# Performance work log

Hardware: AMD Instinct MI355X
Metric: run time of the kernel (lower is better)

Reference implementation:

```python
import jax, jax.numpy as jnp
import numpy as np

N = 192            # image grid size (NxN)
N_SHOTS = 192
N_SAMPLES = 192
TWO_PI = 2.0 * np.pi
PIPE_ITERS = 3     # gpunufft default is ~10; 3 suffices for a CPU-runnable reference


def initialize_2D_radial(n_shots, n_samples):
    """Radial trajectory, k in [-0.5, 0.5), shape (n_shots*n_samples, 2)."""
    angles = np.pi * np.arange(n_shots) / n_shots
    radii = np.linspace(-0.5, 0.5, n_samples, endpoint=False)
    kx = radii[None, :] * np.cos(angles[:, None])
    ky = radii[None, :] * np.sin(angles[:, None])
    return np.stack([kx, ky], axis=-1).reshape(-1, 2).astype(np.float32)


def setup_inputs() -> dict:
    key = jax.random.key(0)
    x = jax.random.normal(key, (2, N, N), dtype=jnp.float32)  # real/imag image
    trajectory = jnp.asarray(initialize_2D_radial(N_SHOTS, N_SAMPLES))  # (M,2)
    return {"x": x, "trajectory": trajectory}


def _mats(traj):
    # Separable NDFT factors: exp(-2pi i k_x * px), exp(-2pi i k_y * py).
    # A: (M, N), B: (M, N); M*N complex64 ~= 57 MB each.
    p = jnp.arange(N, dtype=jnp.float32) - N / 2.0  # centered pixel coords
    A = jnp.exp(-1j * TWO_PI * traj[:, 0:1] * p[None, :])
    B = jnp.exp(-1j * TWO_PI * traj[:, 1:2] * p[None, :])
    return A.astype(jnp.complex64), B.astype(jnp.complex64)


def _op(img, A, B):
    # type-2 NUFFT (exact NDFT): image (N,N) -> kspace (M,)
    t = jnp.einsum('my,xy->mx', B, img)      # contract y first
    return jnp.einsum('mx,mx->m', A, t)


def _adj(d, A, B):
    # type-1 NUFFT adjoint: samples (M,) -> image (N,N)
    return jnp.einsum('mx,my->xy', jnp.conj(A) * d[:, None], jnp.conj(B))


def _pipe_density(A, B):
    # Pipe & Menon iterative density compensation: w <- w / |F F^H w|
    w = jnp.ones(A.shape[0], dtype=jnp.complex64)
    def body(i, w):
        q = _op(_adj(w, A, B), A, B)
        return w / jnp.maximum(jnp.abs(q), 1e-20)
    w = jax.lax.fori_loop(0, PIPE_ITERS, body, w)
    return jnp.abs(w)  # real positive weights


def reference(x, trajectory):
    img = (x[0] + 1j * x[1]).astype(jnp.complex64)  # (N,N) complex image
    A, B = _mats(trajectory)
    # density weights computed from detached trajectory (gpunufft init-time)
    traj_sg = jax.lax.stop_gradient(trajectory)
    Asg, Bsg = _mats(traj_sg)
    w = jax.lax.stop_gradient(_pipe_density(Asg, Bsg))
    kspace = _op(img, A, B)                       # forward NUFFT
    adjoint = _adj(w * kspace, A, B)              # density-compensated adjoint
    return jnp.stack([adjoint.real, adjoint.imag])  # (2,N,N) float32
```

## Files before the change

kernel.cpp:

```cpp
#include <hip/hip_runtime.h>
#include <math.h>


#define MTOT 36864
#define NPIX 192
#define SPLITS 128
#define GRP 64
#define NCH 36
#define PG 64

typedef __attribute__((ext_vector_type(8))) short s16x8;
typedef __attribute__((ext_vector_type(4))) float f32x4;
typedef __attribute__((ext_vector_type(4))) unsigned u32x4;

__device__ __forceinline__ f32x4 mfma_bf16(u32x4 a, u32x4 b, f32x4 c) {
    return __builtin_amdgcn_mfma_f32_16x16x32_bf16(
        __builtin_bit_cast(s16x8, a), __builtin_bit_cast(s16x8, b), c, 0, 0, 0);
}

__device__ __forceinline__ void g2l16(const void* g, void* l) {
    __builtin_amdgcn_global_load_lds(
        (const __attribute__((address_space(1))) void*)g,
        (__attribute__((address_space(3))) void*)l, 16, 0, 0);
}

__device__ __forceinline__ void split_pk(float a, float b, unsigned &hi, unsigned &lo) {
    const unsigned ua = __float_as_uint(a), ub = __float_as_uint(b);
    const unsigned ha = (ua + 0x8000u) & 0xffff0000u;
    const unsigned hb = (ub + 0x8000u) & 0xffff0000u;
    hi = (ha >> 16) | hb;
    const float la = a - __uint_as_float(ha);
    const float lb = b - __uint_as_float(hb);
    lo = ((__float_as_uint(la) + 0x8000u) >> 16) |
         ((__float_as_uint(lb) + 0x8000u) & 0xffff0000u);
}

__device__ __forceinline__ void ksplit(float k, float &kh, float &kl) {
    kh = __uint_as_float(__float_as_uint(k) & 0xfffff000u);
    kl = k - kh;
}
__device__ __forceinline__ float redphase(float kh, float kl, float p) {
    float r = kh * p;
    r -= rintf(r);
    r = fmaf(kl, p, r);
    return r;
}
__device__ __forceinline__ unsigned rot16(unsigned v) {
    return __builtin_amdgcn_alignbit(v, v, 16);
}
__device__ __forceinline__ int swz(int c) {
    return ((c ^ (c >> 2)) & 3) << 2;
}

__global__ void precompP_k(const float* __restrict__ traj, const int comp,
                           unsigned* __restrict__ PS,
                           float* __restrict__ wr, float* __restrict__ wi) {
    const int m = blockIdx.x * 256 + threadIdx.x;
    const int c = blockIdx.y;
    if (c == 0) { wr[m] = 1.f; wi[m] = 0.f; }
    float kh, kl; ksplit(traj[2 * m + comp], kh, kl);
    const float ph = redphase(kh, kl, (float)(c - 96));
    const float co = __builtin_amdgcn_cosf(ph);
    const float si = __builtin_amdgcn_sinf(ph);
    unsigned h, l; split_pk(co, -si, h, l);
    const int mc = m >> 4, mi = (m & 15) ^ swz(c);
    PS[(size_t)mc * 6144 + c * 16 + mi]        = h;
    PS[(size_t)mc * 6144 + 3072 + c * 16 + mi] = l;
}

__global__ void ebuild_k(const float* __restrict__ traj,
                         const float* __restrict__ dr, const float* __restrict__ di,
                         unsigned* __restrict__ ES) {
    const int m = blockIdx.x * 256 + threadIdx.x;
    const int c = blockIdx.y;
    float kh, kl; ksplit(traj[2 * m], kh, kl);
    const float ph = redphase(kh, kl, (float)(c - 96));
    const float co = __builtin_amdgcn_cosf(ph);
    const float si = __builtin_amdgcn_sinf(ph);
    const float dr_ = dr[m], di_ = di[m];
    const float Er = co * dr_ - si * di_;
    const float Ei = co * di_ + si * dr_;
    unsigned h, l; split_pk(Er, Ei, h, l);
    const int mc = m >> 4, mi = (m & 15) ^ swz(c);
    ES[(size_t)mc * 6144 + c * 16 + mi]        = h;
    ES[(size_t)mc * 6144 + 3072 + c * 16 + mi] = l;
}

__global__ __launch_bounds__(256) void adj_gemm_k(
    const unsigned* __restrict__ ES, const unsigned* __restrict__ BS,
    float* __restrict__ outP)
{
    __shared__ unsigned sAB[3][4096];
    const int tid = threadIdx.x;
    const int lane = tid & 63, wid = tid >> 6;
    const int l15 = lane & 15, qd = lane >> 4;
    const int L = blockIdx.x;
    const int xcd = L & 7, j = L >> 3;
    const int g = xcd * (GRP / 8) + j / 9;
    const int tile = j % 9;
    const int bx = tile % 3, by = tile / 3;
    const int wi = wid & 1, wj = wid >> 1;
    const int x0 = bx * 64 + wi * 32, y0 = by * 64 + wj * 32;
    float* outRe = outP + (size_t)g * (2 * MTOT);
    float* outIm = outRe + MTOT;

    f32x4 accRe[2][2], accIm[2][2];
    #pragma unroll
    for (int i = 0; i < 2; ++i)
        #pragma unroll
        for (int j2 = 0; j2 < 2; ++j2) {
            accRe[i][j2] = (f32x4){0.f, 0.f, 0.f, 0.f};
            accIm[i][j2] = (f32x4){0.f, 0.f, 0.f, 0.f};
        }

    const size_t g18 = (size_t)g * 18;
    const int exo = bx * 1024 + tid * 4;
    const int byo = by * 1024 + tid * 4;
    #define STAGE(c, buf)                                                  \
    {                                                                      \
        const size_t id_ = (g18 + (c) + (((c) >= 18) ? 1134 : 0)) * 6144; \
        const unsigned* E0_ = ES + id_;                                    \
        const unsigned* B0_ = BS + id_;                                    \
        g2l16(E0_ + exo,        &sAB[buf][tid * 4]);                       \
        g2l16(E0_ + 3072 + exo, &sAB[buf][1024 + tid * 4]);                \
        g2l16(B0_ + byo,        &sAB[buf][2048 + tid * 4]);                \
        g2l16(B0_ + 3072 + byo, &sAB[buf][3072 + tid * 4]);                \
    }

    int eoff[2], boff[2];
    #pragma unroll
    for (int t = 0; t < 2; ++t) {
        const int cE = wi * 32 + t * 16 + l15;
        eoff[t] = cE * 16 + ((qd ^ ((cE ^ (cE >> 2)) & 3)) << 2);
        const int cB = wj * 32 + t * 16 + l15;
        boff[t] = 2048 + cB * 16 + ((qd ^ ((cB ^ (cB >> 2)) & 3)) << 2);
    }

    STAGE(0, 0);
    STAGE(1, 1);

    int rb = 0;
    for (int ch = 0; ch < NCH; ++ch) {
        if (ch + 1 < NCH) {
            asm volatile("s_waitcnt vmcnt(4)" ::: "memory");
        } else {
            asm volatile("s_waitcnt vmcnt(0)" ::: "memory");
        }
        __builtin_amdgcn_s_barrier();
        if (ch + 2 < NCH) {
            const int wb = (rb + 2 >= 3) ? rb - 1 : rb + 2;
            STAGE(ch + 2, wb);
        }

        const unsigned* sb = &sAB[rb][0];
        u32x4 Eh[2], El[2], PhA[2], PlA[2];
        #pragma unroll
        for (int t = 0; t < 2; ++t) {
            Eh[t]  = *(const u32x4*)(sb + eoff[t]);
            El[t]  = *(const u32x4*)(sb + 1024 + eoff[t]);
            PhA[t] = *(const u32x4*)(sb + boff[t]);
            PlA[t] = *(const u32x4*)(sb + 1024 + boff[t]);
        }
        asm volatile("s_waitcnt lgkmcnt(0)" ::: "memory");
        __builtin_amdgcn_sched_barrier(0);
        __builtin_amdgcn_s_setprio(1);

        #pragma unroll
        for (int sj = 0; sj < 2; ++sj) {
            const u32x4 Ph = PhA[sj], Pl = PlA[sj];
            u32x4 Qh, Ql;
            #pragma unroll
            for (int r = 0; r < 4; ++r) {
                Qh[r] = rot16(Ph[r]) ^ 0x00008000u;
                Ql[r] = rot16(Pl[r]) ^ 0x00008000u;
            }
            #pragma unroll
            for (int si = 0; si < 2; ++si) {
                accRe[si][sj] = mfma_bf16(Eh[si], Ph, accRe[si][sj]);
                accRe[si][sj] = mfma_bf16(Eh[si], Pl, accRe[si][sj]);
                accRe[si][sj] = mfma_bf16(El[si], Ph, accRe[si][sj]);
                accIm[si][sj] = mfma_bf16(Eh[si], Qh, accIm[si][sj]);
                accIm[si][sj] = mfma_bf16(Eh[si], Ql, accIm[si][sj]);
                accIm[si][sj] = mfma_bf16(El[si], Qh, accIm[si][sj]);
            }
        }
        __builtin_amdgcn_s_setprio(0);
        rb = (rb + 1 == 3) ? 0 : rb + 1;
    }
    #undef STAGE

    #pragma unroll
    for (int si = 0; si < 2; ++si)
        #pragma unroll
        for (int sj = 0; sj < 2; ++sj)
            #pragma unroll
            for (int rg = 0; rg < 4; ++rg) {
                const int x = x0 + si * 16 + qd * 4 + rg;
                const int y = y0 + sj * 16 + l15;
                outRe[x * NPIX + y] = accRe[si][sj][rg];
                outIm[x * NPIX + y] = accIm[si][sj][rg];
            }
}

__device__ __forceinline__ void fw_stage_load(const unsigned* __restrict__ Ghi,
                                              const unsigned* __restrict__ Glo,
                                              int tid, int koff, u32x4 st[3]) {
    #pragma unroll
    for (int j = 0; j < 3; ++j) {
        const int li = tid + j * 576;
        if (li < 1536) {
            const int row = li >> 3, pl = (li >> 2) & 1, qt = li & 3;
            const unsigned* src = pl ? Glo : Ghi;
            st[j] = *(const u32x4*)(src + row * 192 + koff + qt * 4);
        }
    }
}
__device__ __forceinline__ void fw_stage_write(unsigned* sb, int tid, const u32x4 st[3]) {
    #pragma unroll
    for (int j = 0; j < 3; ++j) {
        const int li = tid + j * 576;
        if (li < 1536) {
            const int row = li >> 3, pl = (li >> 2) & 1, qt = li & 3;
            *(u32x4*)(sb + pl * 3840 + row * 20 + qt * 4) = st[j];
        }
    }
}

__global__ __launch_bounds__(576) void fwdq_k(
    const float* __restrict__ traj, const unsigned* __restrict__ BS,
    const unsigned* __restrict__ Ghi, const unsigned* __restrict__ Glo,
    float* __restrict__ wre, float* __restrict__ wim,
    const int mode,
    float* __restrict__ qre, float* __restrict__ qim)
{
    __shared__ unsigned sG[2][2 * 3840];
    const int tid = threadIdx.x;
    const int lane = tid & 63, wid = tid >> 6;
    const int l15 = lane & 15, q = lane >> 4;
    const int mc = blockIdx.x * 9 + wid;
    const int m = mc * 16 + l15;
    const float kx = traj[2 * m];
    float kxh, kxl;
    ksplit(kx, kxh, kxl);

    f32x4 tre[12], tim[12];
    #pragma unroll
    for (int i = 0; i < 12; ++i) {
        tre[i] = (f32x4){0.f, 0.f, 0.f, 0.f};
        tim[i] = (f32x4){0.f, 0.f, 0.f, 0.f};
    }

    const unsigned* Bm = BS + (size_t)mc * 6144;
    int od[4];
    #pragma unroll
    for (int r = 0; r < 4; ++r)
        od[r] = (q * 4 + r) * 16 + (l15 ^ (((r ^ q) & 3) << 2));

    unsigned Wh[4], Wl[4];
    #pragma unroll
    for (int r = 0; r < 4; ++r) { Wh[r] = Bm[od[r]]; Wl[r] = Bm[3072 + od[r]]; }

    u32x4 st[3];
    fw_stage_load(Ghi, Glo, tid, 0, st);
    fw_stage_write(&sG[0][0], tid, st);
    __syncthreads();

    for (int ch = 0; ch < 12; ++ch) {
        if (ch < 11) fw_stage_load(Ghi, Glo, tid, (ch + 1) * 16, st);

        u32x4 Ph, Pl, Qh, Ql;
        #pragma unroll
        for (int r = 0; r < 4; ++r) {
            Ph[r] = Wh[r] ^ 0x80000000u;
            Pl[r] = Wl[r] ^ 0x80000000u;
            Qh[r] = rot16(Wh[r]);
            Ql[r] = rot16(Wl[r]);
        }
        unsigned Nh[4], Nl[4];
        if (ch < 11) {
            const unsigned* Bn = Bm + (ch + 1) * 256;
            #pragma unroll
            for (int r = 0; r < 4; ++r) { Nh[r] = Bn[od[r]]; Nl[r] = Bn[3072 + od[r]]; }
        }

        const unsigned* sb = &sG[ch & 1][0];
        #pragma unroll
        for (int si = 0; si < 12; ++si) {
            const int base = (si * 16 + l15) * 20 + q * 4;
            const u32x4 gh = *(const u32x4*)(sb + base);
            const u32x4 gl = *(const u32x4*)(sb + 3840 + base);
            tre[si] = mfma_bf16(gh, Ph, tre[si]);
            tre[si] = mfma_bf16(gh, Pl, tre[si]);
            tre[si] = mfma_bf16(gl, Ph, tre[si]);
            tim[si] = mfma_bf16(gh, Qh, tim[si]);
            tim[si] = mfma_bf16(gh, Ql, tim[si]);
            tim[si] = mfma_bf16(gl, Qh, tim[si]);
        }

        if (ch < 11) {
            fw_stage_write(&sG[(ch + 1) & 1][0], tid, st);
            __syncthreads();
            #pragma unroll
            for (int r = 0; r < 4; ++r) { Wh[r] = Nh[r]; Wl[r] = Nl[r]; }
        }
    }

    float qr = 0.f, qi = 0.f;
    {
        float g = kx * 16.f; g -= rintf(g);
        const float rc = __builtin_amdgcn_cosf(g), rs = __builtin_amdgcn_sinf(g);
        #pragma unroll
        for (int rg = 0; rg < 4; ++rg) {
            const float ph = redphase(kxh, kxl, (float)(q * 4 + rg - 96));
            float c = __builtin_amdgcn_cosf(ph), s = __builtin_amdgcn_sinf(ph);
            #pragma unroll
            for (int si = 0; si < 12; ++si) {
                const float tr = tre[si][rg], ti = tim[si][rg];
                qr += c * tr + s * ti;
                qi += c * ti - s * tr;
                const float nc = c * rc - s * rs, ns = s * rc + c * rs;
                c = nc; s = ns;
            }
        }
    }
    qr += __shfl_xor(qr, 16); qi += __shfl_xor(qi, 16);
    qr += __shfl_xor(qr, 32); qi += __shfl_xor(qi, 32);
    if (lane < 16) {
        if (mode == 0) {
            const float den = fmaxf(sqrtf(qr * qr + qi * qi), 1e-20f);
            wre[m] /= den; wim[m] /= den;
        } else {
            const float sc = sqrtf(wre[m] * wre[m] + wim[m] * wim[m]);
            qre[m] = qr * sc; qim[m] = qi * sc;
        }
    }
}

__global__ void presplit_k(const float* __restrict__ re, const float* __restrict__ im,
                           unsigned* __restrict__ Gh, unsigned* __restrict__ Gl) {
    const int e = blockIdx.x * 256 + threadIdx.x;
    unsigned h, l;
    split_pk(re[e], im[e], h, l);
    Gh[e] = h; Gl[e] = l;
}

__global__ void presplitP_k(const float* __restrict__ outP,
                            unsigned* __restrict__ Gh, unsigned* __restrict__ Gl) {
    const int e = blockIdx.x * 256 + threadIdx.x;
    float re = 0.f, im = 0.f;
    #pragma unroll 8
    for (int g = 0; g < PG; ++g) {
        re += outP[(size_t)g * (2 * MTOT) + e];
        im += outP[(size_t)g * (2 * MTOT) + MTOT + e];
    }
    unsigned h, l;
    split_pk(re, im, h, l);
    Gh[e] = h; Gl[e] = l;
}

__global__ void reduceOut_k(const float* __restrict__ outP, float* __restrict__ out) {
    const int e = blockIdx.x * 256 + threadIdx.x;
    float re = 0.f, im = 0.f;
    #pragma unroll 8
    for (int g = 0; g < PG; ++g) {
        re += outP[(size_t)g * (2 * MTOT) + e];
        im += outP[(size_t)g * (2 * MTOT) + MTOT + e];
    }
    out[e] = re; out[MTOT + e] = im;
}

extern "C" void kernel_launch(void* const* d_in, const int* in_sizes, int n_in,
                              void* d_out, int out_size, void* d_ws, size_t ws_size,
                              hipStream_t stream)
{
    const float* xin  = (const float*)d_in[0];
    const float* traj = (const float*)d_in[1];
    float* out = (float*)d_out;

    char* pb = (char*)d_ws;
    unsigned* BS = (unsigned*)pb; pb += (size_t)2304 * 6144 * 4;
    unsigned* ES = (unsigned*)pb; pb += (size_t)2304 * 6144 * 4;
    float* outP = (float*)pb; pb += (size_t)PG * 2 * MTOT * 4;
    float* wr   = (float*)pb; pb += MTOT * 4;
    float* wi   = (float*)pb; pb += MTOT * 4;
    float* dre  = (float*)pb; pb += MTOT * 4;
    float* dim_ = (float*)pb; pb += MTOT * 4;
    unsigned* Ghi = (unsigned*)pb; pb += MTOT * 4;
    unsigned* Glo = (unsigned*)pb; pb += MTOT * 4;

    precompP_k<<<dim3(MTOT / 256, NPIX), 256, 0, stream>>>(traj, 1, BS, wr, wi);

    for (int it = 0; it < 3; ++it) {
        ebuild_k<<<dim3(MTOT / 256, NPIX), 256, 0, stream>>>(traj, wr, wi, ES);
        adj_gemm_k<<<9 * GRP, 256, 0, stream>>>(ES, BS, outP);
        presplitP_k<<<MTOT / 256, 256, 0, stream>>>(outP, Ghi, Glo);
        fwdq_k<<<256, 576, 0, stream>>>(traj, BS, Ghi, Glo, wr, wi, 0, dre, dim_);
    }

    presplit_k<<<MTOT / 256, 256, 0, stream>>>(xin, xin + MTOT, Ghi, Glo);
    fwdq_k<<<256, 576, 0, stream>>>(traj, BS, Ghi, Glo, wr, wi, 1, dre, dim_);
    ebuild_k<<<dim3(MTOT / 256, NPIX), 256, 0, stream>>>(traj, dre, dim_, ES);
    adj_gemm_k<<<9 * GRP, 256, 0, stream>>>(ES, BS, outP);
    reduceOut_k<<<MTOT / 256, 256, 0, stream>>>(outP, out);
}
```

Baseline: 444.3 us.

## Split forward NUFFT contraction across two blocks with atomic accumulation

The forward q kernel now splits its 12-chunk contraction over the y dimension into two halves, each handled by its own block, which doubles the grid from 256 to 512 blocks. Partial results are combined with atomicAdd into new accumulators that the presplit kernels zero. A separate normq kernel then applies the density normalization or the weight scaling. This is meant to raise occupancy on a GPU with many CUs, at the cost of an extra launch per forward pass and atomic traffic.

```diff
diff --git a/kernel.cpp b/kernel.cpp
--- a/kernel.cpp
+++ b/kernel.cpp
@@ -229,15 +229,15 @@
 __global__ __launch_bounds__(576) void fwdq_k(
     const float* __restrict__ traj, const unsigned* __restrict__ BS,
     const unsigned* __restrict__ Ghi, const unsigned* __restrict__ Glo,
-    float* __restrict__ wre, float* __restrict__ wim,
-    const int mode,
-    float* __restrict__ qre, float* __restrict__ qim)
+    float* __restrict__ qaR, float* __restrict__ qaI)
 {
     __shared__ unsigned sG[2][2 * 3840];
     const int tid = threadIdx.x;
     const int lane = tid & 63, wid = tid >> 6;
     const int l15 = lane & 15, q = lane >> 4;
-    const int mc = blockIdx.x * 9 + wid;
+    const int mcg = blockIdx.x >> 1, half = blockIdx.x & 1;
+    const int c0 = half * 6;
+    const int mc = mcg * 9 + wid;
     const int m = mc * 16 + l15;
     const float kx = traj[2 * m];
     float kxh, kxl;
@@ -257,16 +257,19 @@
         od[r] = (q * 4 + r) * 16 + (l15 ^ (((r ^ q) & 3) << 2));
 
     unsigned Wh[4], Wl[4];
-    #pragma unroll
-    for (int r = 0; r < 4; ++r) { Wh[r] = Bm[od[r]]; Wl[r] = Bm[3072 + od[r]]; }
+    {
+        const unsigned* B0 = Bm + c0 * 256;
+        #pragma unroll
+        for (int r = 0; r < 4; ++r) { Wh[r] = B0[od[r]]; Wl[r] = B0[3072 + od[r]]; }
+    }
 
     u32x4 st[3];
-    fw_stage_load(Ghi, Glo, tid, 0, st);
+    fw_stage_load(Ghi, Glo, tid, c0 * 16, st);
     fw_stage_write(&sG[0][0], tid, st);
     __syncthreads();
 
-    for (int ch = 0; ch < 12; ++ch) {
-        if (ch < 11) fw_stage_load(Ghi, Glo, tid, (ch + 1) * 16, st);
+    for (int ch = 0; ch < 6; ++ch) {
+        if (ch < 5) fw_stage_load(Ghi, Glo, tid, (c0 + ch + 1) * 16, st);
 
         u32x4 Ph, Pl, Qh, Ql;
         #pragma unroll
@@ -277,8 +280,8 @@
             Ql[r] = rot16(Wl[r]);
         }
         unsigned Nh[4], Nl[4];
-        if (ch < 11) {
-            const unsigned* Bn = Bm + (ch + 1) * 256;
+        if (ch < 5) {
+            const unsigned* Bn = Bm + (c0 + ch + 1) * 256;
             #pragma unroll
             for (int r = 0; r < 4; ++r) { Nh[r] = Bn[od[r]]; Nl[r] = Bn[3072 + od[r]]; }
         }
@@ -297,7 +300,7 @@
             tim[si] = mfma_bf16(gl, Qh, tim[si]);
         }
 
-        if (ch < 11) {
+        if (ch < 5) {
             fw_stage_write(&sG[(ch + 1) & 1][0], tid, st);
             __syncthreads();
             #pragma unroll
@@ -326,26 +329,39 @@
     qr += __shfl_xor(qr, 16); qi += __shfl_xor(qi, 16);
     qr += __shfl_xor(qr, 32); qi += __shfl_xor(qi, 32);
     if (lane < 16) {
-        if (mode == 0) {
-            const float den = fmaxf(sqrtf(qr * qr + qi * qi), 1e-20f);
-            wre[m] /= den; wim[m] /= den;
-        } else {
-            const float sc = sqrtf(wre[m] * wre[m] + wim[m] * wim[m]);
-            qre[m] = qr * sc; qim[m] = qi * sc;
-        }
+        atomicAdd(qaR + m, qr);
+        atomicAdd(qaI + m, qi);
+    }
+}
+
+__global__ void normq_k(const float* __restrict__ qaR, const float* __restrict__ qaI,
+                        float* __restrict__ wr, float* __restrict__ wi,
+                        const int mode,
+                        float* __restrict__ dre, float* __restrict__ dim_) {
+    const int m = blockIdx.x * 256 + threadIdx.x;
+    const float qr = qaR[m], qi = qaI[m];
+    if (mode == 0) {
+        const float den = fmaxf(sqrtf(qr * qr + qi * qi), 1e-20f);
+        wr[m] /= den; wi[m] /= den;
+    } else {
+        const float sc = sqrtf(wr[m] * wr[m] + wi[m] * wi[m]);
+        dre[m] = qr * sc; dim_[m] = qi * sc;
     }
 }
 
 __global__ void presplit_k(const float* __restrict__ re, const float* __restrict__ im,
-                           unsigned* __restrict__ Gh, unsigned* __restrict__ Gl) {
+                           unsigned* __restrict__ Gh, unsigned* __restrict__ Gl,
+                           float* __restrict__ qaR, float* __restrict__ qaI) {
     const int e = blockIdx.x * 256 + threadIdx.x;
     unsigned h, l;
     split_pk(re[e], im[e], h, l);
     Gh[e] = h; Gl[e] = l;
+    qaR[e] = 0.f; qaI[e] = 0.f;
 }
 
 __global__ void presplitP_k(const float* __restrict__ outP,
-                            unsigned* __restrict__ Gh, unsigned* __restrict__ Gl) {
+                            unsigned* __restrict__ Gh, unsigned* __restrict__ Gl,
+                            float* __restrict__ qaR, float* __restrict__ qaI) {
     const int e = blockIdx.x * 256 + threadIdx.x;
     float re = 0.f, im = 0.f;
     #pragma unroll 8
@@ -356,6 +372,7 @@
     unsigned h, l;
     split_pk(re, im, h, l);
     Gh[e] = h; Gl[e] = l;
+    qaR[e] = 0.f; qaI[e] = 0.f;
 }
 
 __global__ void reduceOut_k(const float* __restrict__ outP, float* __restrict__ out) {
@@ -387,18 +404,22 @@
     float* dim_ = (float*)pb; pb += MTOT * 4;
     unsigned* Ghi = (unsigned*)pb; pb += MTOT * 4;
     unsigned* Glo = (unsigned*)pb; pb += MTOT * 4;
+    float* qaR = (float*)pb; pb += MTOT * 4;
+    float* qaI = (float*)pb; pb += MTOT * 4;
 
     precompP_k<<<dim3(MTOT / 256, NPIX), 256, 0, stream>>>(traj, 1, BS, wr, wi);
 
     for (int it = 0; it < 3; ++it) {
         ebuild_k<<<dim3(MTOT / 256, NPIX), 256, 0, stream>>>(traj, wr, wi, ES);
         adj_gemm_k<<<9 * GRP, 256, 0, stream>>>(ES, BS, outP);
-        presplitP_k<<<MTOT / 256, 256, 0, stream>>>(outP, Ghi, Glo);
-        fwdq_k<<<256, 576, 0, stream>>>(traj, BS, Ghi, Glo, wr, wi, 0, dre, dim_);
-    }
-
-    presplit_k<<<MTOT / 256, 256, 0, stream>>>(xin, xin + MTOT, Ghi, Glo);
-    fwdq_k<<<256, 576, 0, stream>>>(traj, BS, Ghi, Glo, wr, wi, 1, dre, dim_);
+        presplitP_k<<<MTOT / 256, 256, 0, stream>>>(outP, Ghi, Glo, qaR, qaI);
+        fwdq_k<<<512, 576, 0, stream>>>(traj, BS, Ghi, Glo, qaR, qaI);
+        normq_k<<<MTOT / 256, 256, 0, stream>>>(qaR, qaI, wr, wi, 0, dre, dim_);
+    }
+
+    presplit_k<<<MTOT / 256, 256, 0, stream>>>(xin, xin + MTOT, Ghi, Glo, qaR, qaI);
+    fwdq_k<<<512, 576, 0, stream>>>(traj, BS, Ghi, Glo, qaR, qaI);
+    normq_k<<<MTOT / 256, 256, 0, stream>>>(qaR, qaI, wr, wi, 1, dre, dim_);
     ebuild_k<<<dim3(MTOT / 256, NPIX), 256, 0, stream>>>(traj, dre, dim_, ES);
     adj_gemm_k<<<9 * GRP, 256, 0, stream>>>(ES, BS, outP);
     reduceOut_k<<<MTOT / 256, 256, 0, stream>>>(outP, out);
```

Result: slower. 501.7 us (+12.9%).
